# Kernel optimization log

Hardware: AMD Instinct MI355X
Metric: run time of the kernel (lower is better)

## Reference

```python
import jax, jax.numpy as jnp
import numpy as np

N_NODES, N_EDGES, D_IN, N_GRAPHS = 20000, 320000, 256, 32
H1, C1, H2, C2 = 4, 128, 4, 64


def setup_inputs() -> dict:
    key = jax.random.key(0)
    ks = jax.random.split(key, 24)
    g = lambda k, shape, fan: jax.random.normal(k, shape, jnp.float32) * (1.0 / np.sqrt(fan))
    inp = {
        'x': jax.random.normal(ks[0], (N_NODES, D_IN), jnp.float32),
        'edge_index': jax.random.randint(ks[1], (2, N_EDGES), 0, N_NODES, jnp.int32),
        'batch': jnp.sort(jax.random.randint(ks[2], (N_NODES,), 0, N_GRAPHS, jnp.int32)),
        'edge_attr': jax.random.normal(ks[3], (N_EDGES, 1), jnp.float32),
        # GATConv 1: lin [D_IN, H1*C1], att_src/dst/edge [H1,C1], lin_edge [1,H1*C1], bias [H1*C1]
        'W1': g(ks[4], (D_IN, H1 * C1), D_IN),
        'as1': g(ks[5], (H1, C1), C1),
        'ad1': g(ks[6], (H1, C1), C1),
        'We1': g(ks[7], (1, H1 * C1), 1),
        'ae1': g(ks[8], (H1, C1), C1),
        'b1': jnp.zeros((H1 * C1,), jnp.float32),
        'g1': jnp.ones((H1 * C1,), jnp.float32),
        'be1': jnp.zeros((H1 * C1,), jnp.float32),
        # GATConv 2 (concat=False -> out 64)
        'W2': g(ks[9], (H1 * C1, H2 * C2), H1 * C1),
        'as2': g(ks[10], (H2, C2), C2),
        'ad2': g(ks[11], (H2, C2), C2),
        'We2': g(ks[12], (1, H2 * C2), 1),
        'ae2': g(ks[13], (H2, C2), C2),
        'b2': jnp.zeros((C2,), jnp.float32),
        'g2': jnp.ones((C2,), jnp.float32),
        'be2': jnp.zeros((C2,), jnp.float32),
        'fw1': g(ks[14], (C2, 32), C2),
        'fb1': jnp.zeros((32,), jnp.float32),
        'fw2': g(ks[15], (32, 1), 32),
        'fb2': jnp.zeros((1,), jnp.float32),
    }
    return inp


def _gat(x, src, dst, ea, W, a_s, a_d, We, a_e, bias, H, C, concat, n):
    h = (x @ W).reshape(n, H, C)                         # [N,H,C]
    al_s = jnp.einsum('nhc,hc->nh', h, a_s)              # [N,H]
    al_d = jnp.einsum('nhc,hc->nh', h, a_d)
    e = (ea @ We).reshape(-1, H, C)                      # [E',H,C]
    al_e = jnp.einsum('ehc,hc->eh', e, a_e)
    logits = jax.nn.leaky_relu(al_s[src] + al_d[dst] + al_e, 0.2)  # [E',H]
    m = jax.ops.segment_max(logits, dst, num_segments=n)
    m = jnp.where(jnp.isfinite(m), m, 0.0)
    p = jnp.exp(logits - m[dst])
    denom = jax.ops.segment_sum(p, dst, num_segments=n)
    alpha = p / (denom[dst] + 1e-16)                     # segment softmax
    out = jax.ops.segment_sum(h[src] * alpha[:, :, None], dst, num_segments=n)
    out = out.reshape(n, H * C) if concat else out.mean(axis=1)
    return out + bias


def _bn(x, gamma, beta):
    mu = x.mean(axis=0)
    var = x.var(axis=0)
    return gamma * (x - mu) * jax.lax.rsqrt(var + 1e-5) + beta


def reference(x, edge_index, batch, edge_attr, W1, as1, ad1, We1, ae1, b1, g1, be1,
              W2, as2, ad2, We2, ae2, b2, g2, be2, fw1, fb1, fw2, fb2):
    n = x.shape[0]
    loop = jnp.arange(n, dtype=edge_index.dtype)
    src = jnp.concatenate([edge_index[0], loop])
    dst = jnp.concatenate([edge_index[1], loop])
    # self-loop edge_attr filled with mean (PyG fill_value='mean')
    ea = jnp.concatenate([edge_attr, jnp.broadcast_to(edge_attr.mean(axis=0), (n, edge_attr.shape[1]))])

    h = _gat(x, src, dst, ea, W1, as1, ad1, We1, ae1, b1, H1, C1, True, n)
    h = jax.nn.elu(_bn(h, g1, be1))
    h = _gat(h, src, dst, ea, W2, as2, ad2, We2, ae2, b2, H2, C2, False, n)
    h = jax.nn.elu(_bn(h, g2, be2))

    sums = jax.ops.segment_sum(h, batch, num_segments=N_GRAPHS)
    cnt = jax.ops.segment_sum(jnp.ones((n,), h.dtype), batch, num_segments=N_GRAPHS)
    pooled = sums / jnp.maximum(cnt, 1.0)[:, None]       # global_mean_pool
    # dropout is identity in eval mode
    out = jax.nn.elu(pooled @ fw1 + fb1) @ fw2 + fb2
    return out
```

## Files before the change

kernel.cpp:

```cpp
#include <hip/hip_runtime.h>
#include <hip/hip_bf16.h>

#define N_NODES  20000
#define MPAD     20096
#define N_EDGES  320000
#define N_EP     (N_EDGES + N_NODES)
#define D_IN     256
#define N_GRAPHS 32
#define HH1 4
#define CC1 128
#define HH2 4
#define CC2 64
#define MAXDEG   128

#define XB_OFF      0ull
#define HB1_OFF     10289152ull
#define AGG1_OFF    30867456ull
#define HB2_OFF     51445760ull
#define OUT2_OFF    61734912ull
#define EAF_OFF     66854912ull
#define W1BT_OFF    68134912ull
#define W2BT_OFF    68397056ull
#define CSR_OFF     68659200ull
#define ROWPTR_OFF  71379200ull
#define GSTART_OFF  71459264ull
#define SMALL_OFF   71459520ull
#define SBUF_OFF    71485120ull
#define EAP_OFF     71485184ull
#define ALSP_OFF    71486464ull
#define ALDP_OFF    72129536ull
#define PMU1_OFF    72772608ull
#define PM21_OFF    73296896ull
#define PMU2_OFF    73821184ull
#define PM22_OFF    73886720ull
#define A1_OFF      73952256ull
#define B1_OFF      73954304ull
#define A2_OFF      73956352ull
#define B2_OFF      73956608ull
#define EAACC_OFF   73956864ull
#define DEG_OFF     74600000ull
#define CURS_OFF    74680000ull
#define FLAGZ_OFF   74760000ull
#define ZERO0_START DEG_OFF
#define ZERO0_SIZE  160128ull
#define PP_OFF      74760128ull

#define S_AS1 0
#define S_AD1 512
#define S_WE1 1024
#define S_AE1 1536
#define S_G1  2048
#define S_BE1 2560
#define S_AS2 3072
#define S_AD2 3328
#define S_WE2 3584
#define S_AE2 3840
#define S_G2  4096
#define S_BE2 4160
#define S_FW1 4224
#define S_FB1 6272
#define S_FW2 6304
#define S_FB2 6336

typedef __attribute__((ext_vector_type(8))) short bf8_t;
typedef __attribute__((ext_vector_type(4))) float f4_t;

__device__ __forceinline__ float loadF(const void* p, int i, int fp32) {
    return fp32 ? ((const float*)p)[i]
                : __bfloat162float(((const __hip_bfloat16*)p)[i]);
}

#define DH_DETECT 256
#define HIST_BLOCKS 1329
__global__ void detect_hist(const unsigned short* __restrict__ xr, int* __restrict__ flag,
                            const int* __restrict__ ei, int* __restrict__ deg,
                            const int* __restrict__ batch, int* __restrict__ gstart) {
    int b = blockIdx.x, t = threadIdx.x;
    if (b < DH_DETECT) {
        int i = b * 256 + t;
        unsigned short u = xr[i];
        if ((u & 0x7F80) == 0x7F80) atomicOr(flag, 1);
        return;
    }
    b -= DH_DETECT;
    if (b < HIST_BLOCKS) {
        int e = b * 256 + t;
        if (e >= N_EP) return;
        int d = (e < N_EDGES) ? ei[N_EDGES + e] : e - N_EDGES;
        atomicAdd(&deg[d], 1);
        return;
    }
    int i = (b - HIST_BLOCKS) * 256 + t;
    if (i >= N_NODES) return;
    int bb = batch[i];
    if (i == 0) {
        for (int g = 0; g <= bb; ++g) gstart[g] = 0;
    } else {
        int pb = batch[i - 1];
        for (int g = pb + 1; g <= bb; ++g) gstart[g] = i;
    }
    if (i == N_NODES - 1) {
        for (int g = bb + 1; g <= N_GRAPHS; ++g) gstart[g] = N_NODES;
    }
}

#define PB_XB  5024
#define PB_EAF 313
#define PB_W   512
#define PB_SM  16
#define PREP_BLOCKS (PB_XB + PB_EAF + 2 * PB_W + PB_SM + 1)
__global__ __launch_bounds__(256) void prep(
        const int* __restrict__ flag,
        const void* x, const void* ea, const void* W1, const void* W2,
        const void* as1, const void* ad1, const void* We1, const void* ae1,
        const void* g1, const void* be1, const void* as2, const void* ad2,
        const void* We2, const void* ae2, const void* g2, const void* be2,
        const void* fw1, const void* fb1, const void* fw2, const void* fb2,
        __hip_bfloat16* __restrict__ xb, float* __restrict__ eaf, float* __restrict__ eap,
        __hip_bfloat16* __restrict__ W1bt, __hip_bfloat16* __restrict__ W2bt,
        float* __restrict__ smalls, float* __restrict__ sbuf) {
    __shared__ float shw[4];
    int b = blockIdx.x, t = threadIdx.x;
    int fp32 = flag[0];
    if (b < PB_XB) {
        int base = (b * 256 + t) * 4;
        __hip_bfloat16 tmp[4];
#pragma unroll
        for (int j = 0; j < 4; ++j) {
            int i = base + j;
            float v = (i < N_NODES * D_IN) ? loadF(x, i, fp32) : 0.f;
            tmp[j] = __float2bfloat16(v);
        }
        *(uint2*)&xb[base] = *(uint2*)tmp;
        return;
    }
    b -= PB_XB;
    if (b < PB_EAF) {
        int base = (b * 256 + t) * 4;
        float s = 0.f;
#pragma unroll
        for (int j = 0; j < 4; ++j) {
            int i = base + j;
            if (i < N_EDGES) { float v = loadF(ea, i, fp32); eaf[i] = v; s += v; }
        }
#pragma unroll
        for (int m = 1; m < 64; m <<= 1) s += __shfl_xor(s, m);
        if ((t & 63) == 0) shw[t >> 6] = s;
        __syncthreads();
        if (t == 0) eap[b] = shw[0] + shw[1] + shw[2] + shw[3];
        return;
    }
    b -= PB_EAF;
    if (b < PB_W) {
        int i = b * 256 + t;
        int k = i >> 9, n = i & 511;
        W1bt[(size_t)n * 256 + k] = __float2bfloat16(loadF(W1, i, fp32));
        return;
    }
    b -= PB_W;
    if (b < PB_W) {
        int i = b * 256 + t;
        int k = i >> 8, n = i & 255;
        W2bt[(size_t)n * 512 + k] = __float2bfloat16(loadF(W2, i, fp32));
        return;
    }
    b -= PB_W;
    if (b < PB_SM) {
        const void* srcs[16] = {as1, ad1, We1, ae1, g1, be1, as2, ad2, We2, ae2, g2, be2, fw1, fb1, fw2, fb2};
        const int cnts[16] = {512, 512, 512, 512, 512, 512, 256, 256, 256, 256, 64, 64, 2048, 32, 32, 1};
        const int offs[16] = {S_AS1, S_AD1, S_WE1, S_AE1, S_G1, S_BE1, S_AS2, S_AD2,
                              S_WE2, S_AE2, S_G2, S_BE2, S_FW1, S_FB1, S_FW2, S_FB2};
        for (int i = t; i < cnts[b]; i += 256)
            smalls[offs[b] + i] = loadF(srcs[b], i, fp32);
        return;
    }
    if (t < 4) {
        float s = 0.f;
        for (int c = 0; c < CC1; ++c) s += loadF(We1, t * CC1 + c, fp32) * loadF(ae1, t * CC1 + c, fp32);
        sbuf[t] = s;
    } else if (t < 8) {
        int h = t - 4;
        float s = 0.f;
        for (int c = 0; c < CC2; ++c) s += loadF(We2, h * CC2 + c, fp32) * loadF(ae2, h * CC2 + c, fp32);
        sbuf[4 + h] = s;
    }
}

__global__ __launch_bounds__(1024) void deg_scan(const int* __restrict__ deg, int* __restrict__ rowptr,
                                                 const float* __restrict__ eap, float* __restrict__ ea_acc) {
    __shared__ int part[1024];
    __shared__ float fsh[512];
    int t = threadIdx.x;
    int lo = t * 20;
    int hi = lo + 20; if (hi > N_NODES) hi = N_NODES; if (lo > N_NODES) lo = N_NODES;
    int s = 0;
    for (int i = lo; i < hi; ++i) s += deg[i];
    part[t] = s;
    __syncthreads();
    for (int off = 1; off < 1024; off <<= 1) {
        int u = (t >= off) ? part[t - off] : 0;
        __syncthreads();
        if (t >= off) part[t] += u;
        __syncthreads();
    }
    int run = part[t] - s;
    for (int i = lo; i < hi; ++i) { rowptr[i] = run; run += deg[i]; }
    if (hi == N_NODES && lo < N_NODES) rowptr[N_NODES] = run;
    if (t < 512) fsh[t] = (t < PB_EAF) ? eap[t] : 0.f;
    __syncthreads();
    for (int st = 256; st; st >>= 1) {
        if (t < st) fsh[t] += fsh[t + st];
        __syncthreads();
    }
    if (t == 0) ea_acc[0] = fsh[0];
}

__global__ void edge_scatter(const int* __restrict__ ei, const int* __restrict__ rowptr,
                             int* __restrict__ cursor, int2* __restrict__ csr_se) {
    int e = blockIdx.x * blockDim.x + threadIdx.x;
    if (e >= N_EP) return;
    int s, d;
    if (e < N_EDGES) { s = ei[e]; d = ei[N_EDGES + e]; }
    else { s = d = e - N_EDGES; }
    int pos = rowptr[d] + atomicAdd(&cursor[d], 1);
    csr_se[pos] = make_int2(s, e);
}

__global__ __launch_bounds__(64) void csr_sort_fill(const int* __restrict__ rowptr, int2* __restrict__ cs,
                                                    const float* __restrict__ eaf,
                                                    const float* __restrict__ ea_acc) {
    __shared__ int2 buf[128];
    int d = blockIdx.x;
    int beg = rowptr[d], end = rowptr[d + 1], n = end - beg;
    int lane = threadIdx.x;
    float ea_mean = ea_acc[0] * (1.0f / N_EDGES);
    if (n <= 0) return;
    if (n <= 64) {
        int key = 0x7FFFFFFF, val = 0;
        if (lane < n) { int2 se = cs[beg + lane]; key = se.y; val = se.x; }
        for (int r = 0; r < n; ++r) {
            bool up = ((lane & 1) == (r & 1));
            int partner = up ? lane + 1 : lane - 1;
            bool valid = (partner >= 0) && (partner < 64);
            int pidx = valid ? partner : lane;
            int pk = __shfl(key, pidx);
            int pv = __shfl(val, pidx);
            if (valid && (up ? (pk < key) : (pk > key))) { key = pk; val = pv; }
        }
        if (lane < n) {
            float eav = (key < N_EDGES) ? eaf[key] : ea_mean;
            cs[beg + lane] = make_int2(val, __float_as_int(eav));
        }
        return;
    }
    if (n <= 128) {
        for (int i = lane; i < n; i += 64) buf[i] = cs[beg + i];
        __syncthreads();
        for (int r = 0; r < n; ++r) {
            int i = 2 * lane + (r & 1);
            if (i + 1 < n) {
                int2 a = buf[i], b = buf[i + 1];
                if (a.y > b.y) { buf[i] = b; buf[i + 1] = a; }
            }
            __syncthreads();
        }
        for (int i = lane; i < n; i += 64) {
            int2 se = buf[i];
            float eav = (se.y < N_EDGES) ? eaf[se.y] : ea_mean;
            se.y = __float_as_int(eav);
            cs[beg + i] = se;
        }
        return;
    }
    if (lane == 0) {
        for (int i = beg + 1; i < end; ++i) {
            int2 key = cs[i]; int j = i - 1;
            while (j >= beg && cs[j].y > key.y) { cs[j + 1] = cs[j]; --j; }
            cs[j + 1] = key;
        }
    }
    __syncthreads();
    for (int i = lane; i < n; i += 64) {
        int2 se = cs[beg + i];
        float eav = (se.y < N_EDGES) ? eaf[se.y] : ea_mean;
        se.y = __float_as_int(eav);
        cs[beg + i] = se;
    }
}

__device__ __forceinline__ uint4 bn_elu_pack(uint4 v, const float* __restrict__ a8,
                                             const float* __restrict__ b8) {
    unsigned q[4] = {v.x, v.y, v.z, v.w};
    float4 a0 = *(const float4*)a8, a1 = *(const float4*)(a8 + 4);
    float4 b0 = *(const float4*)b8, b1 = *(const float4*)(b8 + 4);
    float av[8] = {a0.x, a0.y, a0.z, a0.w, a1.x, a1.y, a1.z, a1.w};
    float bv[8] = {b0.x, b0.y, b0.z, b0.w, b1.x, b1.y, b1.z, b1.w};
    __hip_bfloat16 t[8];
#pragma unroll
    for (int k = 0; k < 8; ++k) {
        unsigned u = (k & 1) ? (q[k >> 1] & 0xFFFF0000u) : (q[k >> 1] << 16);
        float y = av[k] * __uint_as_float(u) + bv[k];
        y = y > 0.f ? y : expm1f(y);
        t[k] = __float2bfloat16(y);
    }
    return *(uint4*)t;
}

__global__ __launch_bounds__(256) void gemm_mfma_al(
        const short* __restrict__ A, const short* __restrict__ Bt,
        __hip_bfloat16* __restrict__ Cb, int N, int K,
        float* __restrict__ alsp, float* __restrict__ aldp,
        const float* __restrict__ asv, const float* __restrict__ adv, int cshift,
        const float* __restrict__ bna, const float* __restrict__ bnb) {
    __shared__ short As[128 * 40];
    __shared__ short Bs[64 * 40];
    int t = threadIdx.x;
    int wv = t >> 6, lane = t & 63, quad = lane >> 4, lr = lane & 15;
    int m0 = blockIdx.y * 128, n0 = blockIdx.x * 64;
    f4_t acc[2][4] = {};
    int ra0 = t >> 2, sa0 = t & 3;
    int ra1 = (t + 256) >> 2;
    for (int k0 = 0; k0 < K; k0 += 32) {
        uint4 va0 = *(const uint4*)&A[(size_t)(m0 + ra0) * K + k0 + sa0 * 8];
        uint4 va1 = *(const uint4*)&A[(size_t)(m0 + ra1) * K + k0 + sa0 * 8];
        uint4 vb  = *(const uint4*)&Bt[(size_t)(n0 + ra0) * K + k0 + sa0 * 8];
        if (bna) {
            int j = k0 + sa0 * 8;
            va0 = bn_elu_pack(va0, bna + j, bnb + j);
            va1 = bn_elu_pack(va1, bna + j, bnb + j);
        }
        *(uint4*)&As[ra0 * 40 + sa0 * 8] = va0;
        *(uint4*)&As[ra1 * 40 + sa0 * 8] = va1;
        *(uint4*)&Bs[ra0 * 40 + sa0 * 8] = vb;
        __syncthreads();
        bf8_t a0 = *(const bf8_t*)&As[(wv * 16 + lr) * 40 + quad * 8];
        bf8_t a1 = *(const bf8_t*)&As[((wv + 4) * 16 + lr) * 40 + quad * 8];
#pragma unroll
        for (int nt = 0; nt < 4; ++nt) {
            bf8_t b = *(const bf8_t*)&Bs[(nt * 16 + lr) * 40 + quad * 8];
            acc[0][nt] = __builtin_amdgcn_mfma_f32_16x16x32_bf16(a0, b, acc[0][nt], 0, 0, 0);
            acc[1][nt] = __builtin_amdgcn_mfma_f32_16x16x32_bf16(a1, b, acc[1][nt], 0, 0, 0);
        }
        __syncthreads();
    }
#pragma unroll
    for (int si = 0; si < 2; ++si) {
        int mrow = m0 + (wv + si * 4) * 16 + quad * 4;
#pragma unroll
        for (int nt = 0; nt < 4; ++nt) {
            int col = n0 + nt * 16 + lr;
#pragma unroll
            for (int r = 0; r < 4; ++r)
                Cb[(size_t)(mrow + r) * N + col] = __float2bfloat16(acc[si][nt][r]);
        }
    }
    float asv4[4], adv4[4];
#pragma unroll
    for (int nt = 0; nt < 4; ++nt) {
        asv4[nt] = asv[n0 + nt * 16 + lr];
        adv4[nt] = adv[n0 + nt * 16 + lr];
    }
    int hsel = n0 >> cshift;
    int parity = (n0 >> 6) & ((1 << (cshift - 6)) - 1);
#pragma unroll
    for (int si = 0; si < 2; ++si) {
#pragma unroll
        for (int r = 0; r < 4; ++r) {
            float ps = 0.f, pd = 0.f;
#pragma unroll
            for (int nt = 0; nt < 4; ++nt) {
                ps += acc[si][nt][r] * asv4[nt];
                pd += acc[si][nt][r] * adv4[nt];
            }
#pragma unroll
            for (int m = 1; m < 16; m <<= 1) {
                ps += __shfl_xor(ps, m);
                pd += __shfl_xor(pd, m);
            }
            if (lr == 0) {
                int row = m0 + (wv + si * 4) * 16 + quad * 4 + r;
                alsp[(row * 4 + hsel) * 2 + parity] = ps;
                aldp[(row * 4 + hsel) * 2 + parity] = pd;
            }
        }
    }
}

__device__ __forceinline__ void load_al4(const float* __restrict__ alp, int row, bool np2, float out[4]) {
    const float4* ap = (const float4*)(alp + (size_t)row * 8);
    float4 e0 = ap[0], e1 = ap[1];
    out[0] = e0.x; out[1] = e0.z; out[2] = e1.x; out[3] = e1.z;
    if (np2) { out[0] += e0.y; out[1] += e0.w; out[2] += e1.y; out[3] += e1.w; }
}

__global__ __launch_bounds__(128) void fused_agg1(
        const int* __restrict__ rowptr, const int2* __restrict__ cs,
        const float* __restrict__ alsp, const float* __restrict__ aldp,
        const float* __restrict__ sbuf, const __hip_bfloat16* __restrict__ hb,
        __hip_bfloat16* __restrict__ outb, int nparts) {
    __shared__ float lg[2][MAXDEG * 4];
    __shared__ int   ssrc[2][MAXDEG];
    int wv = threadIdx.x >> 6, t = threadIdx.x & 63;
    int d = blockIdx.x * 2 + wv;
    int beg = rowptr[d], n = rowptr[d + 1] - beg;
    bool fit = (n <= MAXDEG);
    bool np2 = (nparts == 2);
    float adh[4];
    load_al4(aldp, d, np2, adh);
    float sb4[4] = {sbuf[0], sbuf[1], sbuf[2], sbuf[3]};
    float mx[4] = {-INFINITY, -INFINITY, -INFINITY, -INFINITY};
    for (int p = t; p < n; p += 64) {
        int2 se = cs[beg + p];
        float eav = __int_as_float(se.y);
        float l[4];
        load_al4(alsp, se.x, np2, l);
#pragma unroll
        for (int hh = 0; hh < 4; ++hh) {
            float v = l[hh] + adh[hh] + eav * sb4[hh];
            v = v > 0.f ? v : 0.2f * v;
            l[hh] = v;
            mx[hh] = fmaxf(mx[hh], v);
        }
        if (fit) {
            *(float4*)&lg[wv][p * 4] = make_float4(l[0], l[1], l[2], l[3]);
            ssrc[wv][p] = se.x;
        }
    }
#pragma unroll
    for (int m = 1; m < 64; m <<= 1)
#pragma unroll
        for (int hh = 0; hh < 4; ++hh)
            mx[hh] = fmaxf(mx[hh], __shfl_xor(mx[hh], m));
    asm volatile("s_waitcnt lgkmcnt(0)" ::: "memory");
    int h = t >> 4;
    float mh = mx[h];
    float a[8] = {};
    float ds = 0.f;
    const __hip_bfloat16* hrow = hb + 8 * t;
#define ACC8(rr, wt) { \
    unsigned q0 = (rr).x, q1 = (rr).y, q2 = (rr).z, q3 = (rr).w; \
    a[0] += (wt) * __uint_as_float(q0 << 16); a[1] += (wt) * __uint_as_float(q0 & 0xFFFF0000u); \
    a[2] += (wt) * __uint_as_float(q1 << 16); a[3] += (wt) * __uint_as_float(q1 & 0xFFFF0000u); \
    a[4] += (wt) * __uint_as_float(q2 << 16); a[5] += (wt) * __uint_as_float(q2 & 0xFFFF0000u); \
    a[6] += (wt) * __uint_as_float(q3 << 16); a[7] += (wt) * __uint_as_float(q3 & 0xFFFF0000u); }
    if (fit) {
        int p = 0;
        for (; p + 8 <= n; p += 8) {
            int s0 = ssrc[wv][p],     s1 = ssrc[wv][p + 1], s2 = ssrc[wv][p + 2], s3 = ssrc[wv][p + 3];
            int s4 = ssrc[wv][p + 4], s5 = ssrc[wv][p + 5], s6 = ssrc[wv][p + 6], s7 = ssrc[wv][p + 7];
            uint4 r0 = *(const uint4*)&hrow[(size_t)s0 * 512];
            uint4 r1 = *(const uint4*)&hrow[(size_t)s1 * 512];
            uint4 r2 = *(const uint4*)&hrow[(size_t)s2 * 512];
            uint4 r3 = *(const uint4*)&hrow[(size_t)s3 * 512];
            uint4 r4 = *(const uint4*)&hrow[(size_t)s4 * 512];
            uint4 r5 = *(const uint4*)&hrow[(size_t)s5 * 512];
            uint4 r6 = *(const uint4*)&hrow[(size_t)s6 * 512];
            uint4 r7 = *(const uint4*)&hrow[(size_t)s7 * 512];
            float w0 = __expf(lg[wv][p * 4 + h] - mh);
            float w1 = __expf(lg[wv][p * 4 + 4 + h] - mh);
            float w2 = __expf(lg[wv][p * 4 + 8 + h] - mh);
            float w3 = __expf(lg[wv][p * 4 + 12 + h] - mh);
            float w4 = __expf(lg[wv][p * 4 + 16 + h] - mh);
            float w5 = __expf(lg[wv][p * 4 + 20 + h] - mh);
            float w6 = __expf(lg[wv][p * 4 + 24 + h] - mh);
            float w7 = __expf(lg[wv][p * 4 + 28 + h] - mh);
            ds += ((w0 + w1) + (w2 + w3)) + ((w4 + w5) + (w6 + w7));
            ACC8(r0, w0); ACC8(r1, w1); ACC8(r2, w2); ACC8(r3, w3);
            ACC8(r4, w4); ACC8(r5, w5); ACC8(r6, w6); ACC8(r7, w7);
        }
        for (; p + 4 <= n; p += 4) {
            int s0 = ssrc[wv][p], s1 = ssrc[wv][p + 1], s2 = ssrc[wv][p + 2], s3 = ssrc[wv][p + 3];
            uint4 r0 = *(const uint4*)&hrow[(size_t)s0 * 512];
            uint4 r1 = *(const uint4*)&hrow[(size_t)s1 * 512];
            uint4 r2 = *(const uint4*)&hrow[(size_t)s2 * 512];
            uint4 r3 = *(const uint4*)&hrow[(size_t)s3 * 512];
            float w0 = __expf(lg[wv][p * 4 + h] - mh);
            float w1 = __expf(lg[wv][p * 4 + 4 + h] - mh);
            float w2 = __expf(lg[wv][p * 4 + 8 + h] - mh);
            float w3 = __expf(lg[wv][p * 4 + 12 + h] - mh);
            ds += (w0 + w1) + (w2 + w3);
            ACC8(r0, w0); ACC8(r1, w1); ACC8(r2, w2); ACC8(r3, w3);
        }
        for (; p < n; ++p) {
            int s0 = ssrc[wv][p];
            uint4 r0 = *(const uint4*)&hrow[(size_t)s0 * 512];
            float w0 = __expf(lg[wv][p * 4 + h] - mh);
            ds += w0;
            ACC8(r0, w0);
        }
    } else {
        for (int p = 0; p < n; ++p) {
            int2 se = cs[beg + p];
            float eav = __int_as_float(se.y);
            float l4[4];
            load_al4(alsp, se.x, np2, l4);
            float l = l4[h] + adh[h] + eav * sb4[h];
            l = l > 0.f ? l : 0.2f * l;
            float w = __expf(l - mh);
            uint4 r0 = *(const uint4*)&hrow[(size_t)se.x * 512];
            ds += w;
            ACC8(r0, w);
        }
    }
#undef ACC8
    float rdn = 1.0f / (ds + 1e-16f);
    __hip_bfloat16 tmp[8];
#pragma unroll
    for (int j = 0; j < 8; ++j) tmp[j] = __float2bfloat16(a[j] * rdn);
    *(uint4*)&outb[(size_t)d * 512 + 8 * t] = *(uint4*)tmp;
}

__global__ __launch_bounds__(128) void fused_agg2(
        const int* __restrict__ rowptr, const int2* __restrict__ cs,
        const float* __restrict__ alsp, const float* __restrict__ aldp,
        const float* __restrict__ sbuf, const __hip_bfloat16* __restrict__ hb,
        float* __restrict__ out2, int nparts) {
    __shared__ float lg[2][MAXDEG * 4];
    __shared__ int   ssrc[2][MAXDEG];
    int wv = threadIdx.x >> 6, t = threadIdx.x & 63;
    int d = blockIdx.x * 2 + wv;
    int beg = rowptr[d], n = rowptr[d + 1] - beg;
    bool fit = (n <= MAXDEG);
    bool np2 = (nparts == 2);
    float adh[4];
    load_al4(aldp, d, np2, adh);
    float sb4[4] = {sbuf[4], sbuf[5], sbuf[6], sbuf[7]};
    float mx[4] = {-INFINITY, -INFINITY, -INFINITY, -INFINITY};
    for (int p = t; p < n; p += 64) {
        int2 se = cs[beg + p];
        float eav = __int_as_float(se.y);
        float l[4];
        load_al4(alsp, se.x, np2, l);
#pragma unroll
        for (int hh = 0; hh < 4; ++hh) {
            float v = l[hh] + adh[hh] + eav * sb4[hh];
            v = v > 0.f ? v : 0.2f * v;
            l[hh] = v;
            mx[hh] = fmaxf(mx[hh], v);
        }
        if (fit) {
            *(float4*)&lg[wv][p * 4] = make_float4(l[0], l[1], l[2], l[3]);
            ssrc[wv][p] = se.x;
        }
    }
#pragma unroll
    for (int m = 1; m < 64; m <<= 1)
#pragma unroll
        for (int hh = 0; hh < 4; ++hh)
            mx[hh] = fmaxf(mx[hh], __shfl_xor(mx[hh], m));
    asm volatile("s_waitcnt lgkmcnt(0)" ::: "memory");
    int h = t >> 4;
    float mh = mx[h];
    float a4[4] = {};
    float ds = 0.f;
    const __hip_bfloat16* hrow = hb + 4 * t;
#define ACC4(rr, wt) { \
    unsigned q0 = (rr).x, q1 = (rr).y; \
    a4[0] += (wt) * __uint_as_float(q0 << 16); a4[1] += (wt) * __uint_as_float(q0 & 0xFFFF0000u); \
    a4[2] += (wt) * __uint_as_float(q1 << 16); a4[3] += (wt) * __uint_as_float(q1 & 0xFFFF0000u); }
    if (fit) {
        int p = 0;
        for (; p + 8 <= n; p += 8) {
            int s0 = ssrc[wv][p],     s1 = ssrc[wv][p + 1], s2 = ssrc[wv][p + 2], s3 = ssrc[wv][p + 3];
            int s4 = ssrc[wv][p + 4], s5 = ssrc[wv][p + 5], s6 = ssrc[wv][p + 6], s7 = ssrc[wv][p + 7];
            uint2 r0 = *(const uint2*)&hrow[(size_t)s0 * 256];
            uint2 r1 = *(const uint2*)&hrow[(size_t)s1 * 256];
            uint2 r2 = *(const uint2*)&hrow[(size_t)s2 * 256];
            uint2 r3 = *(const uint2*)&hrow[(size_t)s3 * 256];
            uint2 r4 = *(const uint2*)&hrow[(size_t)s4 * 256];
            uint2 r5 = *(const uint2*)&hrow[(size_t)s5 * 256];
            uint2 r6 = *(const uint2*)&hrow[(size_t)s6 * 256];
            uint2 r7 = *(const uint2*)&hrow[(size_t)s7 * 256];
            float w0 = __expf(lg[wv][p * 4 + h] - mh);
            float w1 = __expf(lg[wv][p * 4 + 4 + h] - mh);
            float w2 = __expf(lg[wv][p * 4 + 8 + h] - mh);
            float w3 = __expf(lg[wv][p * 4 + 12 + h] - mh);
            float w4 = __expf(lg[wv][p * 4 + 16 + h] - mh);
            float w5 = __expf(lg[wv][p * 4 + 20 + h] - mh);
            float w6 = __expf(lg[wv][p * 4 + 24 + h] - mh);
            float w7 = __expf(lg[wv][p * 4 + 28 + h] - mh);
            ds += ((w0 + w1) + (w2 + w3)) + ((w4 + w5) + (w6 + w7));
            ACC4(r0, w0); ACC4(r1, w1); ACC4(r2, w2); ACC4(r3, w3);
            ACC4(r4, w4); ACC4(r5, w5); ACC4(r6, w6); ACC4(r7, w7);
        }
        for (; p + 4 <= n; p += 4) {
            int s0 = ssrc[wv][p], s1 = ssrc[wv][p + 1], s2 = ssrc[wv][p + 2], s3 = ssrc[wv][p + 3];
            uint2 r0 = *(const uint2*)&hrow[(size_t)s0 * 256];
            uint2 r1 = *(const uint2*)&hrow[(size_t)s1 * 256];
            uint2 r2 = *(const uint2*)&hrow[(size_t)s2 * 256];
            uint2 r3 = *(const uint2*)&hrow[(size_t)s3 * 256];
            float w0 = __expf(lg[wv][p * 4 + h] - mh);
            float w1 = __expf(lg[wv][p * 4 + 4 + h] - mh);
            float w2 = __expf(lg[wv][p * 4 + 8 + h] - mh);
            float w3 = __expf(lg[wv][p * 4 + 12 + h] - mh);
            ds += (w0 + w1) + (w2 + w3);
            ACC4(r0, w0); ACC4(r1, w1); ACC4(r2, w2); ACC4(r3, w3);
        }
        for (; p < n; ++p) {
            int s0 = ssrc[wv][p];
            uint2 r0 = *(const uint2*)&hrow[(size_t)s0 * 256];
            float w0 = __expf(lg[wv][p * 4 + h] - mh);
            ds += w0;
            ACC4(r0, w0);
        }
    } else {
        for (int p = 0; p < n; ++p) {
            int2 se = cs[beg + p];
            float eav = __int_as_float(se.y);
            float l4[4];
            load_al4(alsp, se.x, np2, l4);
            float l = l4[h] + adh[h] + eav * sb4[h];
            l = l > 0.f ? l : 0.2f * l;
            float w = __expf(l - mh);
            uint2 r0 = *(const uint2*)&hrow[(size_t)se.x * 256];
            ds += w;
            ACC4(r0, w);
        }
    }
#undef ACC4
    float rdn = 1.0f / (ds + 1e-16f);
#pragma unroll
    for (int j = 0; j < 4; ++j) {
        float v = a4[j] * rdn;
        v += __shfl_xor(v, 16);
        v += __shfl_xor(v, 32);
        a4[j] = v * 0.25f;
    }
    if (t < 16)
        *(float4*)&out2[(size_t)d * 64 + 4 * t] = make_float4(a4[0], a4[1], a4[2], a4[3]);
}

__global__ __launch_bounds__(256) void bn_part_b(const __hip_bfloat16* __restrict__ x,
                                                 float* __restrict__ pmu, float* __restrict__ pm2) {
    int t = threadIdx.x, b = blockIdx.x;
    float s0 = 0.f, s20 = 0.f, s1 = 0.f, s21 = 0.f;
    for (int i = b; i < N_NODES; i += gridDim.x) {
        unsigned u = *(const unsigned*)&x[(size_t)i * 512 + 2 * t];
        float v0 = __uint_as_float(u << 16);
        float v1 = __uint_as_float(u & 0xFFFF0000u);
        s0 += v0; s20 += v0 * v0; s1 += v1; s21 += v1 * v1;
    }
    pmu[b * 512 + 2 * t] = s0;     pm2[b * 512 + 2 * t] = s20;
    pmu[b * 512 + 2 * t + 1] = s1; pm2[b * 512 + 2 * t + 1] = s21;
}

__global__ __launch_bounds__(256) void bn_reduce_affine(const float* __restrict__ pmu, const float* __restrict__ pm2,
                                 const float* __restrict__ smalls, int s_g, int s_be,
                                 float* __restrict__ a, float* __restrict__ b, int nch) {
    __shared__ float shs[4][64], sh2[4][64];
    int t = threadIdx.x;
    int cl = t & 63, j = t >> 6;
    int c = blockIdx.x * 64 + cl;
    float s = 0.f, s2 = 0.f;
    for (int bk = j * 64; bk < (j + 1) * 64; ++bk) { s += pmu[bk * nch + c]; s2 += pm2[bk * nch + c]; }
    shs[j][cl] = s; sh2[j][cl] = s2;
    __syncthreads();
    if (j == 0) {
        float st  = ((shs[0][cl] + shs[1][cl]) + (shs[2][cl] + shs[3][cl]));
        float st2 = ((sh2[0][cl] + sh2[1][cl]) + (sh2[2][cl] + sh2[3][cl]));
        float m = st * (1.0f / N_NODES);
        float var = st2 * (1.0f / N_NODES) - m * m;
        float aa = smalls[s_g + c] * rsqrtf(var + 1e-5f);
        a[c] = aa;
        b[c] = smalls[s_be + c] - m * aa;
    }
}

__global__ __launch_bounds__(256) void bn2_stats(const float* __restrict__ x,
                                                 float* __restrict__ pmu, float* __restrict__ pm2) {
    int t = threadIdx.x;
    int c = t & 63, j = t >> 6;
    float ls = 0.f, ls2 = 0.f;
    for (int nd = blockIdx.x * 4 + j; nd < N_NODES; nd += gridDim.x * 4) {
        float v = x[(size_t)nd * 64 + c];
        ls += v; ls2 += v * v;
    }
    __shared__ float shs[4][64], sh2[4][64];
    shs[j][c] = ls; sh2[j][c] = ls2;
    __syncthreads();
    if (j == 0) {
        pmu[blockIdx.x * 64 + c] = shs[0][c] + shs[1][c] + shs[2][c] + shs[3][c];
        pm2[blockIdx.x * 64 + c] = sh2[0][c] + sh2[1][c] + sh2[2][c] + sh2[3][c];
    }
}

__global__ __launch_bounds__(256) void pool_part(const float* __restrict__ x, const int* __restrict__ gstart,
                                                 const float* __restrict__ a2, const float* __restrict__ b2,
                                                 float* __restrict__ pp) {
    int g = blockIdx.x >> 3, ck = blockIdx.x & 7;
    int t = threadIdx.x;
    int c = t & 63, j = t >> 6;
    int beg = gstart[g], end = gstart[g + 1], n = end - beg;
    int cb = beg + (n * ck) / 8, ce = beg + (n * (ck + 1)) / 8;
    float ac = a2[c], bc = b2[c];
    float s = 0.f;
    for (int i = cb + j; i < ce; i += 4) {
        float y = ac * x[(size_t)i * 64 + c] + bc;
        s += (y > 0.f ? y : expm1f(y));
    }
    __shared__ float sh[4][64];
    sh[j][c] = s;
    __syncthreads();
    if (j == 0)
        pp[blockIdx.x * 64 + c] = sh[0][c] + sh[1][c] + sh[2][c] + sh[3][c];
}

__global__ __launch_bounds__(64) void pool_mlp_fin(const float* __restrict__ pp, const int* __restrict__ gstart,
                                                   const float* __restrict__ smalls, const int* __restrict__ flag,
                                                   void* __restrict__ outp) {
    int g = blockIdx.x, t = threadIdx.x;
    __shared__ float pooled[64];
    __shared__ float hsh[32];
    float s = 0.f;
    for (int k = 0; k < 8; ++k) s += pp[(g * 8 + k) * 64 + t];
    int n = gstart[g + 1] - gstart[g];
    pooled[t] = s / fmaxf((float)n, 1.0f);
    __syncthreads();
    if (t < 32) {
        float acc = smalls[S_FB1 + t];
        for (int cc = 0; cc < 64; ++cc)
            acc += pooled[cc] * smalls[S_FW1 + cc * 32 + t];
        hsh[t] = acc > 0.f ? acc : expm1f(acc);
    }
    __syncthreads();
    if (t == 0) {
        float o = smalls[S_FB2];
        for (int k = 0; k < 32; ++k) o += hsh[k] * smalls[S_FW2 + k];
        if (flag[0]) ((float*)outp)[g] = o;
        else ((__hip_bfloat16*)outp)[g] = __float2bfloat16(o);
    }
}

extern "C" void kernel_launch(void* const* d_in, const int* in_sizes, int n_in,
                              void* d_out, int out_size, void* d_ws, size_t ws_size,
                              hipStream_t stream) {
    const void* x    = d_in[0];
    const int* ei    = (const int*)d_in[1];
    const int* batch = (const int*)d_in[2];
    const void* ea   = d_in[3];
    const void* W1   = d_in[4];
    const void* as1  = d_in[5];
    const void* ad1  = d_in[6];
    const void* We1  = d_in[7];
    const void* ae1  = d_in[8];
    const void* g1   = d_in[10];
    const void* be1  = d_in[11];
    const void* W2   = d_in[12];
    const void* as2  = d_in[13];
    const void* ad2  = d_in[14];
    const void* We2  = d_in[15];
    const void* ae2  = d_in[16];
    const void* g2   = d_in[18];
    const void* be2  = d_in[19];
    const void* fw1  = d_in[20];
    const void* fb1  = d_in[21];
    const void* fw2  = d_in[22];
    const void* fb2  = d_in[23];

    char* ws = (char*)d_ws;
    __hip_bfloat16* xb   = (__hip_bfloat16*)(ws + XB_OFF);
    __hip_bfloat16* hb1  = (__hip_bfloat16*)(ws + HB1_OFF);
    __hip_bfloat16* agg1 = (__hip_bfloat16*)(ws + AGG1_OFF);
    __hip_bfloat16* hb2  = (__hip_bfloat16*)(ws + HB2_OFF);
    float* out2   = (float*)(ws + OUT2_OFF);
    float* eaf    = (float*)(ws + EAF_OFF);
    __hip_bfloat16* W1bt = (__hip_bfloat16*)(ws + W1BT_OFF);
    __hip_bfloat16* W2bt = (__hip_bfloat16*)(ws + W2BT_OFF);
    int2*  csr_se = (int2*)(ws + CSR_OFF);
    int*   rowptr = (int*)(ws + ROWPTR_OFF);
    int*   gstart = (int*)(ws + GSTART_OFF);
    float* smalls = (float*)(ws + SMALL_OFF);
    float* sbuf   = (float*)(ws + SBUF_OFF);
    float* eap    = (float*)(ws + EAP_OFF);
    float* alsp   = (float*)(ws + ALSP_OFF);
    float* aldp   = (float*)(ws + ALDP_OFF);
    float* pmu1   = (float*)(ws + PMU1_OFF);
    float* pm21   = (float*)(ws + PM21_OFF);
    float* pmu2   = (float*)(ws + PMU2_OFF);
    float* pm22   = (float*)(ws + PM22_OFF);
    float* a1     = (float*)(ws + A1_OFF);
    float* b1     = (float*)(ws + B1_OFF);
    float* a2     = (float*)(ws + A2_OFF);
    float* b2     = (float*)(ws + B2_OFF);
    float* ea_acc = (float*)(ws + EAACC_OFF);
    float* pp     = (float*)(ws + PP_OFF);
    int*   deg    = (int*)(ws + DEG_OFF);
    int*   cursor = (int*)(ws + CURS_OFF);
    int*   flag   = (int*)(ws + FLAGZ_OFF);

    hipMemsetAsync(ws + ZERO0_START, 0, ZERO0_SIZE, stream);

    detect_hist<<<DH_DETECT + HIST_BLOCKS + 79, 256, 0, stream>>>(
        (const unsigned short*)x, flag, ei, deg, batch, gstart);
    prep<<<PREP_BLOCKS, 256, 0, stream>>>(flag, x, ea, W1, W2,
                                          as1, ad1, We1, ae1, g1, be1, as2, ad2,
                                          We2, ae2, g2, be2, fw1, fb1, fw2, fb2,
                                          xb, eaf, eap, W1bt, W2bt, smalls, sbuf);

    deg_scan<<<1, 1024, 0, stream>>>(deg, rowptr, eap, ea_acc);
    edge_scatter<<<HIST_BLOCKS, 256, 0, stream>>>(ei, rowptr, cursor, csr_se);
    csr_sort_fill<<<N_NODES, 64, 0, stream>>>(rowptr, csr_se, eaf, ea_acc);

    gemm_mfma_al<<<dim3(512 / 64, MPAD / 128), 256, 0, stream>>>(
        (const short*)xb, (const short*)W1bt, hb1, 512, 256,
        alsp, aldp, smalls + S_AS1, smalls + S_AD1, 7, nullptr, nullptr);
    fused_agg1<<<N_NODES / 2, 128, 0, stream>>>(rowptr, csr_se, alsp, aldp, sbuf, hb1, agg1, 2);
    bn_part_b<<<256, 256, 0, stream>>>(agg1, pmu1, pm21);
    bn_reduce_affine<<<8, 256, 0, stream>>>(pmu1, pm21, smalls, S_G1, S_BE1, a1, b1, 512);

    gemm_mfma_al<<<dim3(256 / 64, MPAD / 128), 256, 0, stream>>>(
        (const short*)agg1, (const short*)W2bt, hb2, 256, 512,
        alsp, aldp, smalls + S_AS2, smalls + S_AD2, 6, a1, b1);
    fused_agg2<<<N_NODES / 2, 128, 0, stream>>>(rowptr, csr_se, alsp, aldp, sbuf, hb2, out2, 1);
    bn2_stats<<<256, 256, 0, stream>>>(out2, pmu2, pm22);
    bn_reduce_affine<<<1, 256, 0, stream>>>(pmu2, pm22, smalls, S_G2, S_BE2, a2, b2, 64);

    pool_part<<<N_GRAPHS * 8, 256, 0, stream>>>(out2, gstart, a2, b2, pp);
    pool_mlp_fin<<<N_GRAPHS, 64, 0, stream>>>(pp, gstart, smalls, flag, d_out);
}
```

Measured before the change: 418.2 us.

## Fold edge scatter into GEMM1 launch and move CSR row sort into aggregation

The edge scatter now runs as extra blocks of the first GEMM launch instead of as its own kernel. The separate per-node CSR sort and edge-attribute fill kernel is removed. Each aggregation wave now sorts its row's edges by edge id in shared memory and looks up the edge attribute inline. This saves two kernel launches and a full global read/write pass over the CSR array. In exchange, the per-row sort runs in both aggregation kernels, because the sorted order is not written back for rows that fit in shared memory, and it adds serial latency before each wave's aggregation.

```diff
diff --git a/kernel.cpp b/kernel.cpp
--- a/kernel.cpp
+++ b/kernel.cpp
@@ -215,79 +215,6 @@
     if (t == 0) ea_acc[0] = fsh[0];
 }
 
-__global__ void edge_scatter(const int* __restrict__ ei, const int* __restrict__ rowptr,
-                             int* __restrict__ cursor, int2* __restrict__ csr_se) {
-    int e = blockIdx.x * blockDim.x + threadIdx.x;
-    if (e >= N_EP) return;
-    int s, d;
-    if (e < N_EDGES) { s = ei[e]; d = ei[N_EDGES + e]; }
-    else { s = d = e - N_EDGES; }
-    int pos = rowptr[d] + atomicAdd(&cursor[d], 1);
-    csr_se[pos] = make_int2(s, e);
-}
-
-__global__ __launch_bounds__(64) void csr_sort_fill(const int* __restrict__ rowptr, int2* __restrict__ cs,
-                                                    const float* __restrict__ eaf,
-                                                    const float* __restrict__ ea_acc) {
-    __shared__ int2 buf[128];
-    int d = blockIdx.x;
-    int beg = rowptr[d], end = rowptr[d + 1], n = end - beg;
-    int lane = threadIdx.x;
-    float ea_mean = ea_acc[0] * (1.0f / N_EDGES);
-    if (n <= 0) return;
-    if (n <= 64) {
-        int key = 0x7FFFFFFF, val = 0;
-        if (lane < n) { int2 se = cs[beg + lane]; key = se.y; val = se.x; }
-        for (int r = 0; r < n; ++r) {
-            bool up = ((lane & 1) == (r & 1));
-            int partner = up ? lane + 1 : lane - 1;
-            bool valid = (partner >= 0) && (partner < 64);
-            int pidx = valid ? partner : lane;
-            int pk = __shfl(key, pidx);
-            int pv = __shfl(val, pidx);
-            if (valid && (up ? (pk < key) : (pk > key))) { key = pk; val = pv; }
-        }
-        if (lane < n) {
-            float eav = (key < N_EDGES) ? eaf[key] : ea_mean;
-            cs[beg + lane] = make_int2(val, __float_as_int(eav));
-        }
-        return;
-    }
-    if (n <= 128) {
-        for (int i = lane; i < n; i += 64) buf[i] = cs[beg + i];
-        __syncthreads();
-        for (int r = 0; r < n; ++r) {
-            int i = 2 * lane + (r & 1);
-            if (i + 1 < n) {
-                int2 a = buf[i], b = buf[i + 1];
-                if (a.y > b.y) { buf[i] = b; buf[i + 1] = a; }
-            }
-            __syncthreads();
-        }
-        for (int i = lane; i < n; i += 64) {
-            int2 se = buf[i];
-            float eav = (se.y < N_EDGES) ? eaf[se.y] : ea_mean;
-            se.y = __float_as_int(eav);
-            cs[beg + i] = se;
-        }
-        return;
-    }
-    if (lane == 0) {
-        for (int i = beg + 1; i < end; ++i) {
-            int2 key = cs[i]; int j = i - 1;
-            while (j >= beg && cs[j].y > key.y) { cs[j + 1] = cs[j]; --j; }
-            cs[j + 1] = key;
-        }
-    }
-    __syncthreads();
-    for (int i = lane; i < n; i += 64) {
-        int2 se = cs[beg + i];
-        float eav = (se.y < N_EDGES) ? eaf[se.y] : ea_mean;
-        se.y = __float_as_int(eav);
-        cs[beg + i] = se;
-    }
-}
-
 __device__ __forceinline__ uint4 bn_elu_pack(uint4 v, const float* __restrict__ a8,
                                              const float* __restrict__ b8) {
     unsigned q[4] = {v.x, v.y, v.z, v.w};
@@ -306,17 +233,18 @@
     return *(uint4*)t;
 }
 
-__global__ __launch_bounds__(256) void gemm_mfma_al(
+__device__ __forceinline__ void gemm_body(
         const short* __restrict__ A, const short* __restrict__ Bt,
         __hip_bfloat16* __restrict__ Cb, int N, int K,
         float* __restrict__ alsp, float* __restrict__ aldp,
         const float* __restrict__ asv, const float* __restrict__ adv, int cshift,
-        const float* __restrict__ bna, const float* __restrict__ bnb) {
+        const float* __restrict__ bna, const float* __restrict__ bnb,
+        int bx, int by) {
     __shared__ short As[128 * 40];
     __shared__ short Bs[64 * 40];
     int t = threadIdx.x;
     int wv = t >> 6, lane = t & 63, quad = lane >> 4, lr = lane & 15;
-    int m0 = blockIdx.y * 128, n0 = blockIdx.x * 64;
+    int m0 = by * 128, n0 = bx * 64;
     f4_t acc[2][4] = {};
     int ra0 = t >> 2, sa0 = t & 3;
     int ra1 = (t + 256) >> 2;
@@ -386,6 +314,39 @@
     }
 }
 
+#define G1_BLOCKS 1256
+__global__ __launch_bounds__(256) void gemm1_scatter(
+        const short* __restrict__ A, const short* __restrict__ Bt,
+        __hip_bfloat16* __restrict__ Cb,
+        float* __restrict__ alsp, float* __restrict__ aldp,
+        const float* __restrict__ asv, const float* __restrict__ adv,
+        const int* __restrict__ ei, const int* __restrict__ rowptr,
+        int* __restrict__ cursor, int2* __restrict__ csr_se) {
+    int blk = blockIdx.x;
+    if (blk >= G1_BLOCKS) {
+        int e = (blk - G1_BLOCKS) * 256 + threadIdx.x;
+        if (e >= N_EP) return;
+        int s, dd;
+        if (e < N_EDGES) { s = ei[e]; dd = ei[N_EDGES + e]; }
+        else { s = dd = e - N_EDGES; }
+        int pos = rowptr[dd] + atomicAdd(&cursor[dd], 1);
+        csr_se[pos] = make_int2(s, e);
+        return;
+    }
+    gemm_body(A, Bt, Cb, 512, 256, alsp, aldp, asv, adv, 7, nullptr, nullptr,
+              blk & 7, blk >> 3);
+}
+
+__global__ __launch_bounds__(256) void gemm_mfma_al(
+        const short* __restrict__ A, const short* __restrict__ Bt,
+        __hip_bfloat16* __restrict__ Cb, int N, int K,
+        float* __restrict__ alsp, float* __restrict__ aldp,
+        const float* __restrict__ asv, const float* __restrict__ adv, int cshift,
+        const float* __restrict__ bna, const float* __restrict__ bnb) {
+    gemm_body(A, Bt, Cb, N, K, alsp, aldp, asv, adv, cshift, bna, bnb,
+              blockIdx.x, blockIdx.y);
+}
+
 __device__ __forceinline__ void load_al4(const float* __restrict__ alp, int row, bool np2, float out[4]) {
     const float4* ap = (const float4*)(alp + (size_t)row * 8);
     float4 e0 = ap[0], e1 = ap[1];
@@ -393,37 +354,96 @@
     if (np2) { out[0] += e0.y; out[1] += e0.w; out[2] += e1.y; out[3] += e1.w; }
 }
 
+__device__ __forceinline__ bool wave_sort_row(int2* __restrict__ cs, int beg, int n, int t,
+                                              int2* __restrict__ sbl) {
+    if (n <= 64) {
+        int key = 0x7FFFFFFF, val = 0;
+        if (t < n) { int2 se = cs[beg + t]; key = se.y; val = se.x; }
+        for (int r = 0; r < n; ++r) {
+            bool up = ((t & 1) == (r & 1));
+            int partner = up ? t + 1 : t - 1;
+            bool valid = (partner >= 0) && (partner < 64);
+            int pidx = valid ? partner : t;
+            int pk = __shfl(key, pidx);
+            int pv = __shfl(val, pidx);
+            if (valid && (up ? (pk < key) : (pk > key))) { key = pk; val = pv; }
+        }
+        if (t < n) sbl[t] = make_int2(val, key);
+        asm volatile("s_waitcnt lgkmcnt(0)" ::: "memory");
+        return true;
+    }
+    if (n <= 128) {
+        for (int i = t; i < n; i += 64) sbl[i] = cs[beg + i];
+        asm volatile("s_waitcnt lgkmcnt(0)" ::: "memory");
+        for (int r = 0; r < n; ++r) {
+            int i = 2 * t + (r & 1);
+            if (i + 1 < n) {
+                int2 a = sbl[i], b = sbl[i + 1];
+                if (a.y > b.y) { sbl[i] = b; sbl[i + 1] = a; }
+            }
+            asm volatile("s_waitcnt lgkmcnt(0)" ::: "memory");
+        }
+        return true;
+    }
+    if (t == 0) {
+        for (int i = beg + 1; i < beg + n; ++i) {
+            int2 key2 = cs[i]; int j = i - 1;
+            while (j >= beg && cs[j].y > key2.y) { cs[j + 1] = cs[j]; --j; }
+            cs[j + 1] = key2;
+        }
+    }
+    asm volatile("s_waitcnt vmcnt(0)" ::: "memory");
+    return false;
+}
+
 __global__ __launch_bounds__(128) void fused_agg1(
-        const int* __restrict__ rowptr, const int2* __restrict__ cs,
+        const int* __restrict__ rowptr, int2* __restrict__ cs,
         const float* __restrict__ alsp, const float* __restrict__ aldp,
-        const float* __restrict__ sbuf, const __hip_bfloat16* __restrict__ hb,
+        const float* __restrict__ sbuf, const float* __restrict__ eaf,
+        const float* __restrict__ ea_acc, const __hip_bfloat16* __restrict__ hb,
         __hip_bfloat16* __restrict__ outb, int nparts) {
     __shared__ float lg[2][MAXDEG * 4];
     __shared__ int   ssrc[2][MAXDEG];
+    __shared__ int2  sbl[2][MAXDEG];
     int wv = threadIdx.x >> 6, t = threadIdx.x & 63;
     int d = blockIdx.x * 2 + wv;
     int beg = rowptr[d], n = rowptr[d + 1] - beg;
     bool fit = (n <= MAXDEG);
     bool np2 = (nparts == 2);
+    float ea_mean = ea_acc[0] * (1.0f / N_EDGES);
     float adh[4];
     load_al4(aldp, d, np2, adh);
     float sb4[4] = {sbuf[0], sbuf[1], sbuf[2], sbuf[3]};
     float mx[4] = {-INFINITY, -INFINITY, -INFINITY, -INFINITY};
-    for (int p = t; p < n; p += 64) {
-        int2 se = cs[beg + p];
-        float eav = __int_as_float(se.y);
-        float l[4];
-        load_al4(alsp, se.x, np2, l);
-#pragma unroll
-        for (int hh = 0; hh < 4; ++hh) {
-            float v = l[hh] + adh[hh] + eav * sb4[hh];
-            v = v > 0.f ? v : 0.2f * v;
-            l[hh] = v;
-            mx[hh] = fmaxf(mx[hh], v);
-        }
-        if (fit) {
+    wave_sort_row(cs, beg, n, t, sbl[wv]);
+    if (fit) {
+        for (int p = t; p < n; p += 64) {
+            int2 se = sbl[wv][p];
+            float eav = (se.y < N_EDGES) ? eaf[se.y] : ea_mean;
+            float l[4];
+            load_al4(alsp, se.x, np2, l);
+#pragma unroll
+            for (int hh = 0; hh < 4; ++hh) {
+                float v = l[hh] + adh[hh] + eav * sb4[hh];
+                v = v > 0.f ? v : 0.2f * v;
+                l[hh] = v;
+                mx[hh] = fmaxf(mx[hh], v);
+            }
             *(float4*)&lg[wv][p * 4] = make_float4(l[0], l[1], l[2], l[3]);
             ssrc[wv][p] = se.x;
+        }
+    } else {
+        for (int p = t; p < n; p += 64) {
+            int2 se = cs[beg + p];
+            float eav = (se.y < N_EDGES) ? eaf[se.y] : ea_mean;
+            float l[4];
+            load_al4(alsp, se.x, np2, l);
+#pragma unroll
+            for (int hh = 0; hh < 4; ++hh) {
+                float v = l[hh] + adh[hh] + eav * sb4[hh];
+                v = v > 0.f ? v : 0.2f * v;
+                mx[hh] = fmaxf(mx[hh], v);
+            }
         }
     }
 #pragma unroll
@@ -491,7 +511,7 @@
     } else {
         for (int p = 0; p < n; ++p) {
             int2 se = cs[beg + p];
-            float eav = __int_as_float(se.y);
+            float eav = (se.y < N_EDGES) ? eaf[se.y] : ea_mean;
             float l4[4];
             load_al4(alsp, se.x, np2, l4);
             float l = l4[h] + adh[h] + eav * sb4[h];
@@ -511,36 +531,53 @@
 }
 
 __global__ __launch_bounds__(128) void fused_agg2(
-        const int* __restrict__ rowptr, const int2* __restrict__ cs,
+        const int* __restrict__ rowptr, int2* __restrict__ cs,
         const float* __restrict__ alsp, const float* __restrict__ aldp,
-        const float* __restrict__ sbuf, const __hip_bfloat16* __restrict__ hb,
+        const float* __restrict__ sbuf, const float* __restrict__ eaf,
+        const float* __restrict__ ea_acc, const __hip_bfloat16* __restrict__ hb,
         float* __restrict__ out2, int nparts) {
     __shared__ float lg[2][MAXDEG * 4];
     __shared__ int   ssrc[2][MAXDEG];
+    __shared__ int2  sbl[2][MAXDEG];
     int wv = threadIdx.x >> 6, t = threadIdx.x & 63;
     int d = blockIdx.x * 2 + wv;
     int beg = rowptr[d], n = rowptr[d + 1] - beg;
     bool fit = (n <= MAXDEG);
     bool np2 = (nparts == 2);
+    float ea_mean = ea_acc[0] * (1.0f / N_EDGES);
     float adh[4];
     load_al4(aldp, d, np2, adh);
     float sb4[4] = {sbuf[4], sbuf[5], sbuf[6], sbuf[7]};
     float mx[4] = {-INFINITY, -INFINITY, -INFINITY, -INFINITY};
-    for (int p = t; p < n; p += 64) {
-        int2 se = cs[beg + p];
-        float eav = __int_as_float(se.y);
-        float l[4];
-        load_al4(alsp, se.x, np2, l);
-#pragma unroll
-        for (int hh = 0; hh < 4; ++hh) {
-            float v = l[hh] + adh[hh] + eav * sb4[hh];
-            v = v > 0.f ? v : 0.2f * v;
-            l[hh] = v;
-            mx[hh] = fmaxf(mx[hh], v);
-        }
-        if (fit) {
+    wave_sort_row(cs, beg, n, t, sbl[wv]);
+    if (fit) {
+        for (int p = t; p < n; p += 64) {
+            int2 se = sbl[wv][p];
+            float eav = (se.y < N_EDGES) ? eaf[se.y] : ea_mean;
+            float l[4];
+            load_al4(alsp, se.x, np2, l);
+#pragma unroll
+            for (int hh = 0; hh < 4; ++hh) {
+                float v = l[hh] + adh[hh] + eav * sb4[hh];
+                v = v > 0.f ? v : 0.2f * v;
+                l[hh] = v;
+                mx[hh] = fmaxf(mx[hh], v);
+            }
             *(float4*)&lg[wv][p * 4] = make_float4(l[0], l[1], l[2], l[3]);
             ssrc[wv][p] = se.x;
+        }
+    } else {
+        for (int p = t; p < n; p += 64) {
+            int2 se = cs[beg + p];
+            float eav = (se.y < N_EDGES) ? eaf[se.y] : ea_mean;
+            float l[4];
+            load_al4(alsp, se.x, np2, l);
+#pragma unroll
+            for (int hh = 0; hh < 4; ++hh) {
+                float v = l[hh] + adh[hh] + eav * sb4[hh];
+                v = v > 0.f ? v : 0.2f * v;
+                mx[hh] = fmaxf(mx[hh], v);
+            }
         }
     }
 #pragma unroll
@@ -606,7 +643,7 @@
     } else {
         for (int p = 0; p < n; ++p) {
             int2 se = cs[beg + p];
-            float eav = __int_as_float(se.y);
+            float eav = (se.y < N_EDGES) ? eaf[se.y] : ea_mean;
             float l4[4];
             load_al4(alsp, se.x, np2, l4);
             float l = l4[h] + adh[h] + eav * sb4[h];
@@ -796,22 +833,22 @@
                                           as1, ad1, We1, ae1, g1, be1, as2, ad2,
                                           We2, ae2, g2, be2, fw1, fb1, fw2, fb2,
                                           xb, eaf, eap, W1bt, W2bt, smalls, sbuf);
-
     deg_scan<<<1, 1024, 0, stream>>>(deg, rowptr, eap, ea_acc);
-    edge_scatter<<<HIST_BLOCKS, 256, 0, stream>>>(ei, rowptr, cursor, csr_se);
-    csr_sort_fill<<<N_NODES, 64, 0, stream>>>(rowptr, csr_se, eaf, ea_acc);
-
-    gemm_mfma_al<<<dim3(512 / 64, MPAD / 128), 256, 0, stream>>>(
-        (const short*)xb, (const short*)W1bt, hb1, 512, 256,
-        alsp, aldp, smalls + S_AS1, smalls + S_AD1, 7, nullptr, nullptr);
-    fused_agg1<<<N_NODES / 2, 128, 0, stream>>>(rowptr, csr_se, alsp, aldp, sbuf, hb1, agg1, 2);
+
+    gemm1_scatter<<<G1_BLOCKS + HIST_BLOCKS, 256, 0, stream>>>(
+        (const short*)xb, (const short*)W1bt, hb1,
+        alsp, aldp, smalls + S_AS1, smalls + S_AD1,
+        ei, rowptr, cursor, csr_se);
+    fused_agg1<<<N_NODES / 2, 128, 0, stream>>>(rowptr, csr_se, alsp, aldp, sbuf,
+                                                eaf, ea_acc, hb1, agg1, 2);
     bn_part_b<<<256, 256, 0, stream>>>(agg1, pmu1, pm21);
     bn_reduce_affine<<<8, 256, 0, stream>>>(pmu1, pm21, smalls, S_G1, S_BE1, a1, b1, 512);
 
     gemm_mfma_al<<<dim3(256 / 64, MPAD / 128), 256, 0, stream>>>(
         (const short*)agg1, (const short*)W2bt, hb2, 256, 512,
         alsp, aldp, smalls + S_AS2, smalls + S_AD2, 6, a1, b1);
-    fused_agg2<<<N_NODES / 2, 128, 0, stream>>>(rowptr, csr_se, alsp, aldp, sbuf, hb2, out2, 1);
+    fused_agg2<<<N_NODES / 2, 128, 0, stream>>>(rowptr, csr_se, alsp, aldp, sbuf,
+                                                eaf, ea_acc, hb2, out2, 1);
     bn2_stats<<<256, 256, 0, stream>>>(out2, pmu2, pm22);
     bn_reduce_affine<<<1, 256, 0, stream>>>(pmu2, pm22, smalls, S_G2, S_BE2, a2, b2, 64);
 
```

New measurement: 417.5 us. Within noise of the previous version (-0.2%).
